# Kernel optimization log

Hardware: AMD Instinct MI355X
Metric: run time of the kernel (lower is better)

## Reference

```python
import jax, jax.numpy as jnp
import numpy as np

ALPHA = 2.0
BETA = 50.0
BASE = 0.5
MARGIN = 0.1


def setup_inputs() -> dict:
    key = jax.random.key(0)
    k1, k2 = jax.random.split(key)
    B, D = 8192, 1024
    features1 = jax.random.normal(k1, (B, D), dtype=jnp.float32)
    features2 = jax.random.normal(k2, (B, D), dtype=jnp.float32)
    return {"features1": features1, "features2": features2}


def _ms_loss(sim):
    # sim: [B, B]; diagonal entries are the positive pairs.
    B = sim.shape[0]
    pos = jnp.diagonal(sim)                      # [B]
    off_diag = ~jnp.eye(B, dtype=bool)
    # hard-negative mining: keep off-diagonal entries with sim + margin > pos
    mask = off_diag & (sim + MARGIN > pos[:, None])
    # pos_loss = (1/alpha) * log(1 + exp(-alpha*(pos - base)))  == softplus
    pos_loss = jax.nn.softplus(-ALPHA * (pos - BASE)) / ALPHA   # [B]
    # neg_loss = (1/beta) * log(1 + sum_j exp(beta*(sim_ij - base))) over mined negs;
    # empty set -> sum = 0 -> log1p(0) = 0, matching the len(neg_stats)>0 branch.
    neg_exp = jnp.where(mask, jnp.exp(BETA * (sim - BASE)), 0.0)
    neg_loss = jnp.log1p(jnp.sum(neg_exp, axis=1)) / BETA       # [B]
    return jnp.mean(pos_loss + neg_loss)


def reference(features1, features2):
    f1 = features1 / jnp.linalg.norm(features1, axis=-1, keepdims=True)
    f2 = features2 / jnp.linalg.norm(features2, axis=-1, keepdims=True)
    sim = f1 @ f2.T                               # [B, B]
    loss_i2t = _ms_loss(sim)
    loss_t2i = _ms_loss(sim.T)
    return (loss_i2t + loss_t2i) / 2.0
```

## Files before the change

kernel.cpp:

```cpp
#include <hip/hip_runtime.h>
#include <hip/hip_bf16.h>

#define ALPHA 2.0f
#define BETA 50.0f
#define BASE 0.5f
#define MARGIN 0.1f

constexpr int NB = 8192;
constexpr int ND = 1024;
constexpr int BK = 64;
constexpr int NT = ND / BK;

typedef __attribute__((ext_vector_type(8))) short bf16x8;
typedef __attribute__((ext_vector_type(4))) float f32x4;

#define GLOAD_LDS16(g, l) \
  __builtin_amdgcn_global_load_lds((const __attribute__((address_space(1))) void*)(g), \
                                   (__attribute__((address_space(3))) void*)(l), 16, 0, 0)
#define BAR()    __builtin_amdgcn_s_barrier()
#define WAITV4() asm volatile("s_waitcnt vmcnt(4)" ::: "memory")

static __device__ inline unsigned short f2bf(float x) {
  unsigned int u = __float_as_uint(x);
  unsigned int r = u + 0x7FFFu + ((u >> 16) & 1u);
  return (unsigned short)(r >> 16);
}

__global__ __launch_bounds__(256) void norm_diag_kernel(
    const float* __restrict__ f1, const float* __restrict__ f2,
    unsigned short* __restrict__ f1n, unsigned short* __restrict__ f2n,
    float* __restrict__ diag, float* __restrict__ row_sum,
    float* __restrict__ col_sum)
{
  const int row = blockIdx.x;
  const int tid = threadIdx.x;
  const float4* r1 = (const float4*)(f1 + (size_t)row * ND);
  const float4* r2 = (const float4*)(f2 + (size_t)row * ND);
  float4 a = r1[tid];
  float4 b = r2[tid];
  float ss1 = a.x*a.x + a.y*a.y + a.z*a.z + a.w*a.w;
  float ss2 = b.x*b.x + b.y*b.y + b.z*b.z + b.w*b.w;
  float d12 = a.x*b.x + a.y*b.y + a.z*b.z + a.w*b.w;
  #pragma unroll
  for (int m = 1; m < 64; m <<= 1) {
    ss1 += __shfl_xor(ss1, m);
    ss2 += __shfl_xor(ss2, m);
    d12 += __shfl_xor(d12, m);
  }
  __shared__ float red[3][4];
  const int wid = tid >> 6, lane = tid & 63;
  if (lane == 0) { red[0][wid] = ss1; red[1][wid] = ss2; red[2][wid] = d12; }
  __syncthreads();
  ss1 = red[0][0] + red[0][1] + red[0][2] + red[0][3];
  ss2 = red[1][0] + red[1][1] + red[1][2] + red[1][3];
  d12 = red[2][0] + red[2][1] + red[2][2] + red[2][3];
  const float rn1 = rsqrtf(ss1);
  const float rn2 = rsqrtf(ss2);
  if (tid == 0) diag[row] = d12 * rn1 * rn2;
  if (tid == 1) row_sum[row] = 0.f;
  if (tid == 2) col_sum[row] = 0.f;
  ushort4 o1, o2;
  o1.x = f2bf(a.x * rn1); o1.y = f2bf(a.y * rn1);
  o1.z = f2bf(a.z * rn1); o1.w = f2bf(a.w * rn1);
  o2.x = f2bf(b.x * rn2); o2.y = f2bf(b.y * rn2);
  o2.z = f2bf(b.z * rn2); o2.w = f2bf(b.w * rn2);
  ((ushort4*)f1n)[(size_t)row * 256 + tid] = o1;
  ((ushort4*)f2n)[(size_t)row * 256 + tid] = o2;
}

__global__ __launch_bounds__(512, 2) void simloss_gemm_kernel(
    const unsigned short* __restrict__ f1n, const unsigned short* __restrict__ f2n,
    const float* __restrict__ diag,
    float* __restrict__ row_sum, float* __restrict__ col_sum)
{
  __shared__ unsigned short S[2][2][16384];
  __shared__ float drow[256];
  __shared__ float dcol[256];

  const int tid  = threadIdx.x;
  const int lane = tid & 63;
  const int wid  = tid >> 6;
  const int wm   = wid >> 2;
  const int wn   = wid & 3;

  const int bidl = blockIdx.y * gridDim.x + blockIdx.x;
  const int xcd  = bidl & 7;
  const int i128 = bidl >> 3;
  const int by   = xcd * 4 + (i128 & 3);
  const int bx   = i128 >> 2;
  const int brow = by * 256;
  const int bcol = bx * 256;

  if (tid < 256) drow[tid] = diag[brow + tid];
  else           dcol[tid - 256] = diag[bcol + tid - 256];

  const int c0 = tid, c1 = tid + 512;
  const size_t off0 = (size_t)(c0 >> 3) * ND + (size_t)((((c0 & 7) ^ ((c0 >> 3) & 7))) * 8);
  const size_t off1 = (size_t)(c1 >> 3) * ND + (size_t)((((c1 & 7) ^ ((c1 >> 3) & 7))) * 8);
  const int lo0 = tid * 8, lo1 = tid * 8 + 4096;

  const unsigned short* pA0 = f1n + (size_t)brow * ND;
  const unsigned short* pA1 = pA0 + (size_t)128 * ND;
  const unsigned short* pB0 = f2n + (size_t)bcol * ND;
  const unsigned short* pB1 = pB0 + (size_t)128 * ND;

  #define STAGE(ldsbase, g, kk) do { \
    GLOAD_LDS16((g) + off0 + (kk), (ldsbase) + lo0); \
    GLOAD_LDS16((g) + off1 + (kk), (ldsbase) + lo1); } while (0)

  f32x4 acc[8][4];
  #pragma unroll
  for (int m = 0; m < 8; m++)
    #pragma unroll
    for (int n = 0; n < 4; n++)
      acc[m][n] = (f32x4){0.f, 0.f, 0.f, 0.f};

  const int hi = lane >> 4, l15 = lane & 15;
  const int x7 = l15 & 7;
  const int swz0 = (hi ^ x7) * 8;
  const int swz1 = ((hi + 4) ^ x7) * 8;
  const int abase = (wm * 128 + l15) * 64;
  const int bbase = (wn * 64 + l15) * 64;

  STAGE(&S[0][0][0],    pA0, 0);
  STAGE(&S[0][1][0],    pB0, 0);
  STAGE(&S[0][0][8192], pA1, 0);
  STAGE(&S[0][1][8192], pB1, 0);
  STAGE(&S[1][0][0],    pA0, BK);
  STAGE(&S[1][1][0],    pB0, BK);
  WAITV4();
  BAR();

  bf16x8 a[4][2], b0[2][2], b1[2][2];

  for (int t = 0; t < NT; ++t) {
    const int b  = t & 1, bn = b ^ 1;
    const int k1 = ((t + 1) & 15) * BK;
    const int k2 = ((t + 2) & 15) * BK;
    const unsigned short* PA = &S[b][0][0];
    const unsigned short* PB = &S[b][1][0];

    #pragma unroll
    for (int m = 0; m < 4; ++m) {
      a[m][0] = *(const bf16x8*)&PA[abase + m * 1024 + swz0];
      a[m][1] = *(const bf16x8*)&PA[abase + m * 1024 + swz1];
    }
    #pragma unroll
    for (int n = 0; n < 2; ++n) {
      b0[n][0] = *(const bf16x8*)&PB[bbase + n * 1024 + swz0];
      b0[n][1] = *(const bf16x8*)&PB[bbase + n * 1024 + swz1];
    }
    STAGE(&S[bn][0][8192], pA1, k1);
    BAR();
    __builtin_amdgcn_s_setprio(1);
    #pragma unroll
    for (int k = 0; k < 2; ++k)
      #pragma unroll
      for (int m = 0; m < 4; ++m)
        #pragma unroll
        for (int n = 0; n < 2; ++n)
          acc[m][n] = __builtin_amdgcn_mfma_f32_16x16x32_bf16(a[m][k], b0[n][k], acc[m][n], 0, 0, 0);
    __builtin_amdgcn_s_setprio(0);
    BAR();

    #pragma unroll
    for (int n = 0; n < 2; ++n) {
      b1[n][0] = *(const bf16x8*)&PB[bbase + (n + 2) * 1024 + swz0];
      b1[n][1] = *(const bf16x8*)&PB[bbase + (n + 2) * 1024 + swz1];
    }
    STAGE(&S[bn][1][8192], pB1, k1);
    BAR();
    __builtin_amdgcn_s_setprio(1);
    #pragma unroll
    for (int k = 0; k < 2; ++k)
      #pragma unroll
      for (int m = 0; m < 4; ++m)
        #pragma unroll
        for (int n = 0; n < 2; ++n)
          acc[m][n + 2] = __builtin_amdgcn_mfma_f32_16x16x32_bf16(a[m][k], b1[n][k], acc[m][n + 2], 0, 0, 0);
    __builtin_amdgcn_s_setprio(0);
    BAR();

    #pragma unroll
    for (int m = 0; m < 4; ++m) {
      a[m][0] = *(const bf16x8*)&PA[abase + (m + 4) * 1024 + swz0];
      a[m][1] = *(const bf16x8*)&PA[abase + (m + 4) * 1024 + swz1];
    }
    STAGE(&S[b][1][0], pB0, k2);
    BAR();
    __builtin_amdgcn_s_setprio(1);
    #pragma unroll
    for (int k = 0; k < 2; ++k)
      #pragma unroll
      for (int m = 0; m < 4; ++m)
        #pragma unroll
        for (int n = 0; n < 2; ++n)
          acc[m + 4][n] = __builtin_amdgcn_mfma_f32_16x16x32_bf16(a[m][k], b0[n][k], acc[m + 4][n], 0, 0, 0);
    __builtin_amdgcn_s_setprio(0);
    BAR();

    STAGE(&S[b][0][0], pA0, k2);
    WAITV4();
    BAR();
    __builtin_amdgcn_s_setprio(1);
    #pragma unroll
    for (int k = 0; k < 2; ++k)
      #pragma unroll
      for (int m = 0; m < 4; ++m)
        #pragma unroll
        for (int n = 0; n < 2; ++n)
          acc[m + 4][n + 2] = __builtin_amdgcn_mfma_f32_16x16x32_bf16(a[m][k], b1[n][k], acc[m + 4][n + 2], 0, 0, 0);
    __builtin_amdgcn_s_setprio(0);
    BAR();
  }

  const int cgrp = lane >> 4;
  const int c15  = lane & 15;
  float rp[8][4];
  float cp[4];
  #pragma unroll
  for (int m = 0; m < 8; m++)
    #pragma unroll
    for (int r = 0; r < 4; r++) rp[m][r] = 0.f;
  #pragma unroll
  for (int n = 0; n < 4; n++) cp[n] = 0.f;

  #pragma unroll
  for (int n = 0; n < 4; n++) {
    const int ct   = wn * 64 + n * 16 + c15;
    const int gcol = bcol + ct;
    const float dc = dcol[ct];
    #pragma unroll
    for (int m = 0; m < 8; m++) {
      #pragma unroll
      for (int r = 0; r < 4; r++) {
        const int rt   = wm * 128 + m * 16 + cgrp * 4 + r;
        const int grow = brow + rt;
        const float s  = acc[m][n][r];
        const float e  = __expf(BETA * (s - BASE));
        const float dr = drow[rt];
        const bool off = (grow != gcol);
        if (off && (s + MARGIN > dr)) rp[m][r] += e;
        if (off && (s + MARGIN > dc)) cp[n] += e;
      }
    }
  }
  #pragma unroll
  for (int m = 0; m < 8; m++) {
    #pragma unroll
    for (int r = 0; r < 4; r++) {
      float v = rp[m][r];
      v += __shfl_xor(v, 1); v += __shfl_xor(v, 2);
      v += __shfl_xor(v, 4); v += __shfl_xor(v, 8);
      if (c15 == 0) {
        const int rt = wm * 128 + m * 16 + cgrp * 4 + r;
        atomicAdd(&row_sum[brow + rt], v);
      }
    }
  }
  #pragma unroll
  for (int n = 0; n < 4; n++) {
    float v = cp[n];
    v += __shfl_xor(v, 16); v += __shfl_xor(v, 32);
    if (cgrp == 0) {
      const int ct = wn * 64 + n * 16 + c15;
      atomicAdd(&col_sum[bcol + ct], v);
    }
  }
  #undef STAGE
}

__global__ __launch_bounds__(1024) void finalize_kernel(
    const float* __restrict__ diag, const float* __restrict__ row_sum,
    const float* __restrict__ col_sum, float* __restrict__ out)
{
  const int tid = threadIdx.x;
  float sp = 0.f, sr = 0.f, sc = 0.f;
  for (int i = tid; i < NB; i += 1024) {
    const float pos = diag[i];
    const float x = -ALPHA * (pos - BASE);
    sp += (fmaxf(x, 0.f) + log1pf(__expf(-fabsf(x)))) / ALPHA;
    sr += log1pf(row_sum[i]);
    sc += log1pf(col_sum[i]);
  }
  #pragma unroll
  for (int m = 1; m < 64; m <<= 1) {
    sp += __shfl_xor(sp, m);
    sr += __shfl_xor(sr, m);
    sc += __shfl_xor(sc, m);
  }
  __shared__ float red[3][16];
  const int wid = tid >> 6, lane = tid & 63;
  if (lane == 0) { red[0][wid] = sp; red[1][wid] = sr; red[2][wid] = sc; }
  __syncthreads();
  if (tid == 0) {
    sp = 0.f; sr = 0.f; sc = 0.f;
    #pragma unroll
    for (int w = 0; w < 16; w++) { sp += red[0][w]; sr += red[1][w]; sc += red[2][w]; }
    out[0] = sp / (float)NB + (sr + sc) / (2.f * BETA * (float)NB);
  }
}

extern "C" void kernel_launch(void* const* d_in, const int* in_sizes, int n_in,
                              void* d_out, int out_size, void* d_ws, size_t ws_size,
                              hipStream_t stream) {
  const float* f1 = (const float*)d_in[0];
  const float* f2 = (const float*)d_in[1];
  float* out = (float*)d_out;

  char* ws = (char*)d_ws;
  unsigned short* f1n = (unsigned short*)ws;
  unsigned short* f2n = (unsigned short*)(ws + (size_t)16 * 1024 * 1024);
  float* diag    = (float*)(ws + (size_t)32 * 1024 * 1024);
  float* row_sum = diag + NB;
  float* col_sum = row_sum + NB;

  norm_diag_kernel<<<NB, 256, 0, stream>>>(f1, f2, f1n, f2n, diag, row_sum, col_sum);

  dim3 grid(NB / 256, NB / 256);
  simloss_gemm_kernel<<<grid, 512, 0, stream>>>(f1n, f2n, diag, row_sum, col_sum);

  finalize_kernel<<<1, 1024, 0, stream>>>(diag, row_sum, col_sum, out);
}
```

Measured before the change: 273.0 us.

## Prefetch next-tile LDS fragments during MFMA phases with double-buffered registers

Restructures the GEMM main loop so the A-low and B0 fragments for the next K tile are read from LDS while the current tile's last MFMA quadrants run. Registers are ping-ponged across a 2x-unrolled loop, and the order of the global-to-LDS stages and vmcnt waits is changed. Scheduling barriers pin the issue order. The goal is to hide LDS read latency behind matrix work, at the cost of extra registers that may lower occupancy or cause spills, and tighter LDS hazard ordering.

Result: slower. 294.9 us (+8.0%).

```diff
diff --git a/kernel.cpp b/kernel.cpp
--- a/kernel.cpp
+++ b/kernel.cpp
@@ -18,7 +18,8 @@
   __builtin_amdgcn_global_load_lds((const __attribute__((address_space(1))) void*)(g), \
                                    (__attribute__((address_space(3))) void*)(l), 16, 0, 0)
 #define BAR()    __builtin_amdgcn_s_barrier()
-#define WAITV4() asm volatile("s_waitcnt vmcnt(4)" ::: "memory")
+#define WAITV(N) asm volatile("s_waitcnt vmcnt(" #N ")" ::: "memory")
+#define SCHEDB() __builtin_amdgcn_sched_barrier(0)
 
 static __device__ inline unsigned short f2bf(float x) {
   unsigned int u = __float_as_uint(x);
@@ -122,97 +123,95 @@
   const int abase = (wm * 128 + l15) * 64;
   const int bbase = (wn * 64 + l15) * 64;
 
+  bf16x8 aL0[4][2], aL1[4][2];
+  bf16x8 aH[4][2];
+  bf16x8 b0A[2][2], b0B[2][2];
+  bf16x8 b1f[2][2];
+
+  #define RD_ALO(dst, P) do { _Pragma("unroll") \
+    for (int m = 0; m < 4; ++m) { \
+      dst[m][0] = *(const bf16x8*)&(P)[abase + m * 1024 + swz0]; \
+      dst[m][1] = *(const bf16x8*)&(P)[abase + m * 1024 + swz1]; } } while (0)
+  #define RD_AHI(dst, P) do { _Pragma("unroll") \
+    for (int m = 0; m < 4; ++m) { \
+      dst[m][0] = *(const bf16x8*)&(P)[abase + (m + 4) * 1024 + swz0]; \
+      dst[m][1] = *(const bf16x8*)&(P)[abase + (m + 4) * 1024 + swz1]; } } while (0)
+  #define RD_B0(dst, P) do { _Pragma("unroll") \
+    for (int n = 0; n < 2; ++n) { \
+      dst[n][0] = *(const bf16x8*)&(P)[bbase + n * 1024 + swz0]; \
+      dst[n][1] = *(const bf16x8*)&(P)[bbase + n * 1024 + swz1]; } } while (0)
+  #define RD_B1(dst, P) do { _Pragma("unroll") \
+    for (int n = 0; n < 2; ++n) { \
+      dst[n][0] = *(const bf16x8*)&(P)[bbase + (n + 2) * 1024 + swz0]; \
+      dst[n][1] = *(const bf16x8*)&(P)[bbase + (n + 2) * 1024 + swz1]; } } while (0)
+
+  #define MFMAQ(MO, NO, A, B) do { \
+    __builtin_amdgcn_s_setprio(1); \
+    _Pragma("unroll") \
+    for (int k = 0; k < 2; ++k) \
+      _Pragma("unroll") \
+      for (int m = 0; m < 4; ++m) \
+        _Pragma("unroll") \
+        for (int n = 0; n < 2; ++n) \
+          acc[m + MO][n + NO] = __builtin_amdgcn_mfma_f32_16x16x32_bf16( \
+              A[m][k], B[n][k], acc[m + MO][n + NO], 0, 0, 0); \
+    __builtin_amdgcn_s_setprio(0); } while (0)
+
   STAGE(&S[0][0][0],    pA0, 0);
   STAGE(&S[0][1][0],    pB0, 0);
   STAGE(&S[0][0][8192], pA1, 0);
   STAGE(&S[0][1][8192], pB1, 0);
+  STAGE(&S[1][1][0],    pB0, BK);
   STAGE(&S[1][0][0],    pA0, BK);
-  STAGE(&S[1][1][0],    pB0, BK);
-  WAITV4();
+  WAITV(4);
   BAR();
-
-  bf16x8 a[4][2], b0[2][2], b1[2][2];
-
-  for (int t = 0; t < NT; ++t) {
-    const int b  = t & 1, bn = b ^ 1;
-    const int k1 = ((t + 1) & 15) * BK;
-    const int k2 = ((t + 2) & 15) * BK;
-    const unsigned short* PA = &S[b][0][0];
-    const unsigned short* PB = &S[b][1][0];
-
-    #pragma unroll
-    for (int m = 0; m < 4; ++m) {
-      a[m][0] = *(const bf16x8*)&PA[abase + m * 1024 + swz0];
-      a[m][1] = *(const bf16x8*)&PA[abase + m * 1024 + swz1];
-    }
-    #pragma unroll
-    for (int n = 0; n < 2; ++n) {
-      b0[n][0] = *(const bf16x8*)&PB[bbase + n * 1024 + swz0];
-      b0[n][1] = *(const bf16x8*)&PB[bbase + n * 1024 + swz1];
-    }
-    STAGE(&S[bn][0][8192], pA1, k1);
-    BAR();
-    __builtin_amdgcn_s_setprio(1);
-    #pragma unroll
-    for (int k = 0; k < 2; ++k)
-      #pragma unroll
-      for (int m = 0; m < 4; ++m)
-        #pragma unroll
-        for (int n = 0; n < 2; ++n)
-          acc[m][n] = __builtin_amdgcn_mfma_f32_16x16x32_bf16(a[m][k], b0[n][k], acc[m][n], 0, 0, 0);
-    __builtin_amdgcn_s_setprio(0);
-    BAR();
-
-    #pragma unroll
-    for (int n = 0; n < 2; ++n) {
-      b1[n][0] = *(const bf16x8*)&PB[bbase + (n + 2) * 1024 + swz0];
-      b1[n][1] = *(const bf16x8*)&PB[bbase + (n + 2) * 1024 + swz1];
-    }
-    STAGE(&S[bn][1][8192], pB1, k1);
-    BAR();
-    __builtin_amdgcn_s_setprio(1);
-    #pragma unroll
-    for (int k = 0; k < 2; ++k)
-      #pragma unroll
-      for (int m = 0; m < 4; ++m)
-        #pragma unroll
-        for (int n = 0; n < 2; ++n)
-          acc[m][n + 2] = __builtin_amdgcn_mfma_f32_16x16x32_bf16(a[m][k], b1[n][k], acc[m][n + 2], 0, 0, 0);
-    __builtin_amdgcn_s_setprio(0);
-    BAR();
-
-    #pragma unroll
-    for (int m = 0; m < 4; ++m) {
-      a[m][0] = *(const bf16x8*)&PA[abase + (m + 4) * 1024 + swz0];
-      a[m][1] = *(const bf16x8*)&PA[abase + (m + 4) * 1024 + swz1];
-    }
-    STAGE(&S[b][1][0], pB0, k2);
-    BAR();
-    __builtin_amdgcn_s_setprio(1);
-    #pragma unroll
-    for (int k = 0; k < 2; ++k)
-      #pragma unroll
-      for (int m = 0; m < 4; ++m)
-        #pragma unroll
-        for (int n = 0; n < 2; ++n)
-          acc[m + 4][n] = __builtin_amdgcn_mfma_f32_16x16x32_bf16(a[m][k], b0[n][k], acc[m + 4][n], 0, 0, 0);
-    __builtin_amdgcn_s_setprio(0);
-    BAR();
-
-    STAGE(&S[b][0][0], pA0, k2);
-    WAITV4();
-    BAR();
-    __builtin_amdgcn_s_setprio(1);
-    #pragma unroll
-    for (int k = 0; k < 2; ++k)
-      #pragma unroll
-      for (int m = 0; m < 4; ++m)
-        #pragma unroll
-        for (int n = 0; n < 2; ++n)
-          acc[m + 4][n + 2] = __builtin_amdgcn_mfma_f32_16x16x32_bf16(a[m][k], b1[n][k], acc[m + 4][n + 2], 0, 0, 0);
-    __builtin_amdgcn_s_setprio(0);
-    BAR();
-  }
+  SCHEDB();
+  RD_ALO(aL0, (&S[0][0][0]));
+  RD_B0(b0A, (&S[0][1][0]));
+
+  #define BODY(BI, NI, CAL, NAL, CB0, NB0, t) do { \
+    const int k1 = (((t) + 1) & 15) * BK; \
+    const int k2 = (((t) + 2) & 15) * BK; \
+    const unsigned short* PA  = &S[BI][0][0]; \
+    const unsigned short* PB  = &S[BI][1][0]; \
+    const unsigned short* PAn = &S[NI][0][0]; \
+    const unsigned short* PBn = &S[NI][1][0]; \
+     \
+    RD_B1(b1f, PB); \
+    STAGE(&S[NI][1][8192], pB1, k1); \
+    SCHEDB(); \
+    BAR(); \
+    MFMAQ(0, 0, CAL, CB0); \
+    BAR(); \
+     \
+    RD_AHI(aH, PA); \
+    STAGE(&S[NI][0][8192], pA1, k1); \
+    SCHEDB(); \
+    BAR(); \
+    MFMAQ(0, 2, CAL, b1f); \
+    BAR(); \
+     \
+    STAGE(&S[BI][1][0], pB0, k2); \
+    WAITV(4); \
+    BAR(); \
+    SCHEDB(); \
+    RD_B0(NB0, PBn); \
+    MFMAQ(4, 0, aH, CB0); \
+    BAR(); \
+     \
+    STAGE(&S[BI][0][0], pA0, k2); \
+    WAITV(4); \
+    BAR(); \
+    SCHEDB(); \
+    RD_ALO(NAL, PAn); \
+    MFMAQ(4, 2, aH, b1f); \
+    BAR(); } while (0)
+
+  for (int u = 0; u < NT / 2; ++u) {
+    BODY(0, 1, aL0, aL1, b0A, b0B, 2 * u);
+    BODY(1, 0, aL1, aL0, b0B, b0A, 2 * u + 1);
+  }
+  #undef BODY
 
   const int cgrp = lane >> 4;
   const int c15  = lane & 15;
```
